# Optimization experiments

Hardware: AMD Instinct MI355X
Metric: run time of the kernel (lower is better)

## Reference

```python
import jax, jax.numpy as jnp
import numpy as np
from jax import lax

NX, NY, H = 128, 128, 1.0
N_ITER = 320          # ~2.5*(NX+NY): enough for one-cell-per-iter wavefront propagation
NUM_STATION = 24
NUM_EVENT = 2000
NUM_PICKS = 200000
INF = 1.0e6


def setup_inputs() -> dict:
    key = jax.random.key(0)
    ks = jax.random.split(key, 8)
    # velocities (km/s): vp ~ U[5,6], vs = vp/1.73 (Poisson solid)
    vp = 5.0 + jax.random.uniform(ks[0], (NX, NY), dtype=jnp.float32)
    vs = vp / 1.73
    scale = jnp.array([(NX - 1) * H, (NY - 1) * H, 0.0], dtype=jnp.float32)
    station_loc = jax.random.uniform(ks[1], (NUM_STATION, 3), dtype=jnp.float32) * scale
    event_loc = jax.random.uniform(ks[2], (NUM_EVENT, 3), dtype=jnp.float32) * scale
    event_time = jax.random.normal(ks[3], (NUM_EVENT, 1), dtype=jnp.float32)
    pick_station = jax.random.randint(ks[4], (NUM_PICKS,), 0, NUM_STATION)
    pick_phase = jax.random.randint(ks[5], (NUM_PICKS,), 0, 2)  # 0=P, 1=S
    pick_event = jax.random.randint(ks[6], (NUM_PICKS,), 0, NUM_EVENT)
    phase_time = 20.0 + jax.random.normal(ks[7], (NUM_PICKS,), dtype=jnp.float32)
    return dict(vp=vp, vs=vs, station_loc=station_loc, event_loc=event_loc,
                event_time=event_time, pick_station=pick_station,
                pick_phase=pick_phase, pick_event=pick_event, phase_time=phase_time)


def eikonal_solve(f, ix, iy):
    """2D eikonal |grad u| = f, point source at grid (ix,iy).
    Vectorized Jacobi iteration of the upwind Godunov local solver
    (same fixed point as the C++ fast-sweeping op)."""
    fh = f * H
    src = jnp.zeros((NX, NY), bool).at[ix, iy].set(True)
    u0 = jnp.where(src, 0.0, INF).astype(f.dtype)

    def body(u, _):
        up = jnp.pad(u, 1, constant_values=INF)
        a = jnp.minimum(up[:-2, 1:-1], up[2:, 1:-1])   # min x-neighbors
        b = jnp.minimum(up[1:-1, :-2], up[1:-1, 2:])   # min y-neighbors
        d = jnp.abs(a - b)
        one_sided = jnp.minimum(a, b) + fh
        two_sided = 0.5 * (a + b + jnp.sqrt(jnp.maximum(2.0 * fh * fh - d * d, 0.0)))
        cand = jnp.where(d >= fh, one_sided, two_sided)
        un = jnp.where(src, 0.0, jnp.minimum(u, cand))
        return un, None

    u, _ = lax.scan(body, u0, None, length=N_ITER)
    return u


def _forward(vp, vs, station_loc, event_loc, event_time,
             pick_station, pick_phase, pick_event, phase_time):
    # station grid indices: ix = round(station_x / h)
    ix = jnp.clip(jnp.round(station_loc[:, 0] / H), 0, NX - 1).astype(jnp.int32)
    iy = jnp.clip(jnp.round(station_loc[:, 1] / H), 0, NY - 1).astype(jnp.int32)
    solve_all = jax.vmap(eikonal_solve, in_axes=(None, 0, 0))
    Tp = solve_all(1.0 / vp, ix, iy)          # [S, NX, NY]
    Ts = solve_all(1.0 / vs, ix, iy)          # [S, NX, NY]
    T = jnp.stack([Tp, Ts])                    # [2, S, NX, NY]

    # bilinear interpolation of travel-time table at event locations (per pick)
    x = event_loc[pick_event, 0]
    y = event_loc[pick_event, 1]
    ir0 = jnp.clip(jnp.floor(x / H), 0, NX - 2).astype(jnp.int32)
    iz0 = jnp.clip(jnp.floor(y / H), 0, NY - 2).astype(jnp.int32)
    xc = jnp.clip(x, 0.0, (NX - 1) * H)
    yc = jnp.clip(y, 0.0, (NY - 1) * H)
    r0 = ir0.astype(xc.dtype) * H
    z0 = iz0.astype(yc.dtype) * H
    r1 = r0 + H
    z1 = z0 + H
    ph, st = pick_phase, pick_station
    Q00 = T[ph, st, ir0, iz0]
    Q01 = T[ph, st, ir0, iz0 + 1]
    Q10 = T[ph, st, ir0 + 1, iz0]
    Q11 = T[ph, st, ir0 + 1, iz0 + 1]
    tt = (Q00 * (r1 - xc) * (z1 - yc) + Q10 * (xc - r0) * (z1 - yc)
          + Q01 * (r1 - xc) * (yc - z0) + Q11 * (xc - r0) * (yc - z0)) / (H * H)

    at = event_time[pick_event, 0] + tt        # predicted arrival time, [NUM_PICKS]

    # loss = sum over (station, phase) groups of per-group MSE (matches groupby loop)
    gid = st * 2 + ph
    sq = (at - phase_time) ** 2
    sse = jax.ops.segment_sum(sq, gid, num_segments=2 * NUM_STATION)
    cnt = jax.ops.segment_sum(jnp.ones_like(sq), gid, num_segments=2 * NUM_STATION)
    loss = jnp.sum(sse / jnp.maximum(cnt, 1.0))
    return at, loss


def reference(vp, vs, station_loc, event_loc, event_time,
              pick_station, pick_phase, pick_event, phase_time):
    return _forward(vp, vs, station_loc, event_loc, event_time,
                    pick_station, pick_phase, pick_event, phase_time)
```

## Files before the change

### kernel.cpp

```cpp
#include <hip/hip_runtime.h>

#define NXg   128
#define NYg   128
#define NSTA  24
#define NPICK 200000
#define INFV  1.0e6f
#define TS    8
#define TG    16
#define MAXO  200

__device__ __forceinline__ float fsqrt_fast(float x) {
#if __has_builtin(__builtin_amdgcn_sqrtf)
  return __builtin_amdgcn_sqrtf(x);
#else
  float r; asm("v_sqrt_f32 %0, %1" : "=v"(r) : "v"(x)); return r;
#endif
}


template<int DR, int DC>
__device__ __forceinline__ void gs_pass(
    float (&u)[TS][TS], const float (&fh)[TS][TS], const float (&t2)[TS][TS],
    const float (&tpa)[TS], const float (&bta)[TS],
    const float (&lfa)[TS], const float (&rga)[TS], int &chg)
{
#pragma unroll
  for (int rr = 0; rr < TS; rr++) {
    const int r = (DR > 0) ? rr : (TS - 1 - rr);
#pragma unroll
    for (int cc = 0; cc < TS; cc++) {
      const int c = (DC > 0) ? cc : (TS - 1 - cc);
      const float up = (r == 0)      ? tpa[c] : u[r - 1][c];
      const float dn = (r == TS - 1) ? bta[c] : u[r + 1][c];
      const float lf = (c == 0)      ? lfa[r] : u[r][c - 1];
      const float rt = (c == TS - 1) ? rga[r] : u[r][c + 1];
      const float a  = fminf(up, dn);
      const float b  = fminf(lf, rt);
      const float dd = a - b;
      const float w  = fh[r][c];
      const float s  = fmaxf(__builtin_fmaf(-dd, dd, t2[r][c]), 0.0f);
      const float tw = 0.5f * ((a + b) + fsqrt_fast(s));
      const float on = fminf(a, b) + w;
      const float cand = (fabsf(dd) >= w) ? on : tw;
      const float old = u[r][c];
      chg |= (cand < old);
      u[r][c] = fminf(old, cand);
    }
  }
}

__global__ __launch_bounds__(256, 1) void eik_kernel(
    const float* __restrict__ vp, const float* __restrict__ vs,
    const float* __restrict__ station_loc, float* __restrict__ tab)
{
  __shared__ float eT[TG * TG][TS];
  __shared__ float eB[TG * TG][TS];
  __shared__ float eL[TG * TG][TS];
  __shared__ float eR[TG * TG][TS];
  __shared__ int flg[TG + 2][TG + 2];

  const int t    = threadIdx.x;
  const int wv   = t >> 6;
  const int lane = t & 63;
  const int ti = (wv >> 1) * 8 + (lane >> 3);
  const int tj = (wv & 1) * 8 + (lane & 7);
  const int tid = ti * TG + tj;
  const int fi = ti + 1, fj = tj + 1;

  const int blk = blockIdx.x;
  const int st = blk % NSTA;
  const int ph = blk / NSTA;
  const float* __restrict__ v = ph ? vs : vp;

  for (int i = t; i < (TG + 2) * (TG + 2); i += 256) {
    const int r = i / (TG + 2), c = i % (TG + 2);
    (&flg[0][0])[i] = (r >= 1 && r <= TG && c >= 1 && c <= TG) ? 1 : 0;
  }

  const float sx = station_loc[st * 3 + 0];
  const float sy = station_loc[st * 3 + 1];
  int ix = (int)rintf(sx); ix = ix < 0 ? 0 : (ix > NXg - 1 ? NXg - 1 : ix);
  int iy = (int)rintf(sy); iy = iy < 0 ? 0 : (iy > NYg - 1 ? NYg - 1 : iy);

  const int r0 = ti * TS, c0 = tj * TS;
  float u[TS][TS], fh[TS][TS], t2[TS][TS];
#pragma unroll
  for (int r = 0; r < TS; r++) {
    const float4 v0 = *reinterpret_cast<const float4*>(&v[(r0 + r) * NYg + c0]);
    const float4 v1 = *reinterpret_cast<const float4*>(&v[(r0 + r) * NYg + c0 + 4]);
    fh[r][0] = 1.0f / v0.x; fh[r][1] = 1.0f / v0.y;
    fh[r][2] = 1.0f / v0.z; fh[r][3] = 1.0f / v0.w;
    fh[r][4] = 1.0f / v1.x; fh[r][5] = 1.0f / v1.y;
    fh[r][6] = 1.0f / v1.z; fh[r][7] = 1.0f / v1.w;
#pragma unroll
    for (int c = 0; c < TS; c++) {
      t2[r][c] = (2.0f * fh[r][c]) * fh[r][c];
      u[r][c] = ((r0 + r) == ix && (c0 + c) == iy) ? 0.0f : INFV;
    }
  }

  auto publish = [&]() {
    *reinterpret_cast<float4*>(&eT[tid][0]) = make_float4(u[0][0], u[0][1], u[0][2], u[0][3]);
    *reinterpret_cast<float4*>(&eT[tid][4]) = make_float4(u[0][4], u[0][5], u[0][6], u[0][7]);
    *reinterpret_cast<float4*>(&eB[tid][0]) = make_float4(u[7][0], u[7][1], u[7][2], u[7][3]);
    *reinterpret_cast<float4*>(&eB[tid][4]) = make_float4(u[7][4], u[7][5], u[7][6], u[7][7]);
    *reinterpret_cast<float4*>(&eL[tid][0]) = make_float4(u[0][0], u[1][0], u[2][0], u[3][0]);
    *reinterpret_cast<float4*>(&eL[tid][4]) = make_float4(u[4][0], u[5][0], u[6][0], u[7][0]);
    *reinterpret_cast<float4*>(&eR[tid][0]) = make_float4(u[0][7], u[1][7], u[2][7], u[3][7]);
    *reinterpret_cast<float4*>(&eR[tid][4]) = make_float4(u[4][7], u[5][7], u[6][7], u[7][7]);
  };

  publish();
  __syncthreads();

  for (int outer = 0; outer < MAXO; outer++) {
    const int nb = flg[fi][fj]
                 | flg[fi - 1][fj] | flg[fi + 1][fj]
                 | flg[fi][fj - 1] | flg[fi][fj + 1];
    int chg = 0;
    if (__any(nb)) {
      float tpa[TS], bta[TS], lfa[TS], rga[TS];
      {
        float4 h0 = make_float4(INFV, INFV, INFV, INFV), h1 = h0;
        if (ti > 0) {
          h0 = *reinterpret_cast<const float4*>(&eB[tid - TG][0]);
          h1 = *reinterpret_cast<const float4*>(&eB[tid - TG][4]);
        }
        tpa[0] = h0.x; tpa[1] = h0.y; tpa[2] = h0.z; tpa[3] = h0.w;
        tpa[4] = h1.x; tpa[5] = h1.y; tpa[6] = h1.z; tpa[7] = h1.w;
      }
      {
        float4 h0 = make_float4(INFV, INFV, INFV, INFV), h1 = h0;
        if (ti < TG - 1) {
          h0 = *reinterpret_cast<const float4*>(&eT[tid + TG][0]);
          h1 = *reinterpret_cast<const float4*>(&eT[tid + TG][4]);
        }
        bta[0] = h0.x; bta[1] = h0.y; bta[2] = h0.z; bta[3] = h0.w;
        bta[4] = h1.x; bta[5] = h1.y; bta[6] = h1.z; bta[7] = h1.w;
      }
      {
        float4 h0 = make_float4(INFV, INFV, INFV, INFV), h1 = h0;
        if (tj > 0) {
          h0 = *reinterpret_cast<const float4*>(&eR[tid - 1][0]);
          h1 = *reinterpret_cast<const float4*>(&eR[tid - 1][4]);
        }
        lfa[0] = h0.x; lfa[1] = h0.y; lfa[2] = h0.z; lfa[3] = h0.w;
        lfa[4] = h1.x; lfa[5] = h1.y; lfa[6] = h1.z; lfa[7] = h1.w;
      }
      {
        float4 h0 = make_float4(INFV, INFV, INFV, INFV), h1 = h0;
        if (tj < TG - 1) {
          h0 = *reinterpret_cast<const float4*>(&eL[tid + 1][0]);
          h1 = *reinterpret_cast<const float4*>(&eL[tid + 1][4]);
        }
        rga[0] = h0.x; rga[1] = h0.y; rga[2] = h0.z; rga[3] = h0.w;
        rga[4] = h1.x; rga[5] = h1.y; rga[6] = h1.z; rga[7] = h1.w;
      }

      gs_pass<+1, +1>(u, fh, t2, tpa, bta, lfa, rga, chg);
      gs_pass<+1, -1>(u, fh, t2, tpa, bta, lfa, rga, chg);
      gs_pass<-1, +1>(u, fh, t2, tpa, bta, lfa, rga, chg);
      gs_pass<-1, -1>(u, fh, t2, tpa, bta, lfa, rga, chg);
    }

    __syncthreads();

    flg[fi][fj] = chg;
    if (chg) publish();

    if (!__syncthreads_or(chg)) break;
  }

  float* __restrict__ To = tab + (size_t)(ph * NSTA + st) * NXg * NYg;
#pragma unroll
  for (int r = 0; r < TS; r++) {
    *reinterpret_cast<float4*>(&To[(r0 + r) * NYg + c0]) =
        make_float4(u[r][0], u[r][1], u[r][2], u[r][3]);
    *reinterpret_cast<float4*>(&To[(r0 + r) * NYg + c0 + 4]) =
        make_float4(u[r][4], u[r][5], u[r][6], u[r][7]);
  }
}

__global__ void picks_kernel(
    const float* __restrict__ evloc, const float* __restrict__ evtime,
    const int* __restrict__ pst, const int* __restrict__ pph,
    const int* __restrict__ pev, const float* __restrict__ ptime,
    const float* __restrict__ tab, float* __restrict__ out,
    float* __restrict__ acc)
{
  __shared__ float lsse[2 * NSTA];
  __shared__ float lcnt[2 * NSTA];
  if (threadIdx.x < 2 * NSTA) { lsse[threadIdx.x] = 0.0f; lcnt[threadIdx.x] = 0.0f; }
  __syncthreads();

  int i = blockIdx.x * blockDim.x + threadIdx.x;
  if (i < NPICK) {
    int e = pev[i], s = pst[i], p = pph[i];
    float x = evloc[e * 3 + 0];
    float y = evloc[e * 3 + 1];
    int ir0 = (int)floorf(x); ir0 = ir0 < 0 ? 0 : (ir0 > NXg - 2 ? NXg - 2 : ir0);
    int iz0 = (int)floorf(y); iz0 = iz0 < 0 ? 0 : (iz0 > NYg - 2 ? NYg - 2 : iz0);
    float xc = fminf(fmaxf(x, 0.0f), (float)(NXg - 1));
    float yc = fminf(fmaxf(y, 0.0f), (float)(NYg - 1));
    float r0f = (float)ir0, z0f = (float)iz0;
    float r1 = r0f + 1.0f, z1 = z0f + 1.0f;

    const float* Tb = tab + (size_t)(p * NSTA + s) * NXg * NYg;
    float Q00 = Tb[ir0 * NYg + iz0];
    float Q01 = Tb[ir0 * NYg + iz0 + 1];
    float Q10 = Tb[(ir0 + 1) * NYg + iz0];
    float Q11 = Tb[(ir0 + 1) * NYg + iz0 + 1];
    float tt = Q00 * (r1 - xc) * (z1 - yc) + Q10 * (xc - r0f) * (z1 - yc)
             + Q01 * (r1 - xc) * (yc - z0f) + Q11 * (xc - r0f) * (yc - z0f);
    float at = evtime[e] + tt;
    out[i] = at;

    float dq = at - ptime[i];
    int g = s * 2 + p;
    atomicAdd(&lsse[g], dq * dq);
    atomicAdd(&lcnt[g], 1.0f);
  }
  __syncthreads();
  if (threadIdx.x < 2 * NSTA) {
    atomicAdd(&acc[threadIdx.x], lsse[threadIdx.x]);
    atomicAdd(&acc[2 * NSTA + threadIdx.x], lcnt[threadIdx.x]);
  }
}

__global__ void loss_kernel(const float* __restrict__ acc, float* __restrict__ out)
{
  int l = threadIdx.x;
  float v = 0.0f;
  if (l < 2 * NSTA) v = acc[l] / fmaxf(acc[2 * NSTA + l], 1.0f);
#pragma unroll
  for (int o = 32; o > 0; o >>= 1) v += __shfl_down(v, o, 64);
  if (l == 0) out[NPICK] = v;
}

extern "C" void kernel_launch(void* const* d_in, const int* in_sizes, int n_in,
                              void* d_out, int out_size, void* d_ws, size_t ws_size,
                              hipStream_t stream)
{
  const float* vp           = (const float*)d_in[0];
  const float* vs           = (const float*)d_in[1];
  const float* station_loc  = (const float*)d_in[2];
  const float* event_loc    = (const float*)d_in[3];
  const float* event_time   = (const float*)d_in[4];
  const int*   pick_station = (const int*)d_in[5];
  const int*   pick_phase   = (const int*)d_in[6];
  const int*   pick_event   = (const int*)d_in[7];
  const float* phase_time   = (const float*)d_in[8];

  float* out = (float*)d_out;
  float* acc = (float*)d_ws;
  float* tab = acc + 256;

  hipMemsetAsync(d_ws, 0, 96 * sizeof(float), stream);

  eik_kernel<<<2 * NSTA, 256, 0, stream>>>(vp, vs, station_loc, tab);

  picks_kernel<<<(NPICK + 255) / 256, 256, 0, stream>>>(
      event_loc, event_time, pick_station, pick_phase, pick_event, phase_time,
      tab, out, acc);

  loss_kernel<<<1, 64, 0, stream>>>(acc, out);
}
```

Measured before the change: 320.7 us.

## Split each tile iteration into two alternating sweep pairs with a two-iteration activity mask

Each outer iteration now runs two opposite-direction Gauss-Seidel sweeps instead of all four, alternating between the (+,+)/(-,-) and (+,-)/(-,+) pairs. Halo edges are therefore exchanged between tiles twice as often. A 2-bit history mask keeps a tile active if it or a neighbour changed in either of the last two iterations, and the change flag is only computed on the first sweep of each pair. The sqrt clamp is dropped because the one-sided branch is chosen whenever the argument could go negative. The aim is to spread the wavefront across tiles in fewer total sweeps, at the cost of more barriers and shared-memory publishes per sweep.

```diff
diff --git a/kernel.cpp b/kernel.cpp
--- a/kernel.cpp
+++ b/kernel.cpp
@@ -7,7 +7,7 @@
 #define INFV  1.0e6f
 #define TS    8
 #define TG    16
-#define MAXO  200
+#define MAXH  400
 
 __device__ __forceinline__ float fsqrt_fast(float x) {
 #if __has_builtin(__builtin_amdgcn_sqrtf)
@@ -18,7 +18,7 @@
 }
 
 
-template<int DR, int DC>
+template<int DR, int DC, bool CHK>
 __device__ __forceinline__ void gs_pass(
     float (&u)[TS][TS], const float (&fh)[TS][TS], const float (&t2)[TS][TS],
     const float (&tpa)[TS], const float (&bta)[TS],
@@ -38,12 +38,12 @@
       const float b  = fminf(lf, rt);
       const float dd = a - b;
       const float w  = fh[r][c];
-      const float s  = fmaxf(__builtin_fmaf(-dd, dd, t2[r][c]), 0.0f);
+      const float s  = __builtin_fmaf(-dd, dd, t2[r][c]);
       const float tw = 0.5f * ((a + b) + fsqrt_fast(s));
       const float on = fminf(a, b) + w;
       const float cand = (fabsf(dd) >= w) ? on : tw;
       const float old = u[r][c];
-      chg |= (cand < old);
+      if (CHK) chg |= (cand < old);
       u[r][c] = fminf(old, cand);
     }
   }
@@ -57,7 +57,7 @@
   __shared__ float eB[TG * TG][TS];
   __shared__ float eL[TG * TG][TS];
   __shared__ float eR[TG * TG][TS];
-  __shared__ int flg[TG + 2][TG + 2];
+  __shared__ int msk[TG + 2][TG + 2];
 
   const int t    = threadIdx.x;
   const int wv   = t >> 6;
@@ -74,7 +74,7 @@
 
   for (int i = t; i < (TG + 2) * (TG + 2); i += 256) {
     const int r = i / (TG + 2), c = i % (TG + 2);
-    (&flg[0][0])[i] = (r >= 1 && r <= TG && c >= 1 && c <= TG) ? 1 : 0;
+    (&msk[0][0])[i] = (r >= 1 && r <= TG && c >= 1 && c <= TG) ? 3 : 0;
   }
 
   const float sx = station_loc[st * 3 + 0];
@@ -113,12 +113,12 @@
   publish();
   __syncthreads();
 
-  for (int outer = 0; outer < MAXO; outer++) {
-    const int nb = flg[fi][fj]
-                 | flg[fi - 1][fj] | flg[fi + 1][fj]
-                 | flg[fi][fj - 1] | flg[fi][fj + 1];
+  for (int hg = 0; hg < MAXH; hg++) {
+    const int nbm = msk[fi][fj]
+                  | msk[fi - 1][fj] | msk[fi + 1][fj]
+                  | msk[fi][fj - 1] | msk[fi][fj + 1];
     int chg = 0;
-    if (__any(nb)) {
+    if (__any(nbm)) {
       float tpa[TS], bta[TS], lfa[TS], rga[TS];
       {
         float4 h0 = make_float4(INFV, INFV, INFV, INFV), h1 = h0;
@@ -157,15 +157,18 @@
         rga[4] = h1.x; rga[5] = h1.y; rga[6] = h1.z; rga[7] = h1.w;
       }
 
-      gs_pass<+1, +1>(u, fh, t2, tpa, bta, lfa, rga, chg);
-      gs_pass<+1, -1>(u, fh, t2, tpa, bta, lfa, rga, chg);
-      gs_pass<-1, +1>(u, fh, t2, tpa, bta, lfa, rga, chg);
-      gs_pass<-1, -1>(u, fh, t2, tpa, bta, lfa, rga, chg);
+      if ((hg & 1) == 0) {
+        gs_pass<+1, +1, true >(u, fh, t2, tpa, bta, lfa, rga, chg);
+        gs_pass<-1, -1, false>(u, fh, t2, tpa, bta, lfa, rga, chg);
+      } else {
+        gs_pass<+1, -1, true >(u, fh, t2, tpa, bta, lfa, rga, chg);
+        gs_pass<-1, +1, false>(u, fh, t2, tpa, bta, lfa, rga, chg);
+      }
     }
 
     __syncthreads();
 
-    flg[fi][fj] = chg;
+    msk[fi][fj] = ((msk[fi][fj] << 1) | chg) & 3;
     if (chg) publish();
 
     if (!__syncthreads_or(chg)) break;
```

Result: no change. 326.0 us (+1.7%).

## Order sweeps away from source per wave and skip passes once wave converges

Applied to the files above, without the earlier changes.

Each wave picks a Gauss-Seidel sweep order whose first pass runs away from the source, based on its quadrant relative to the source cell. After each directional pass the wave checks with __any whether anything changed and skips the remaining passes if not. The clamp before the sqrt is removed, since the two-sided branch is only selected when the argument is non-negative. This aims to cut redundant sweep work near convergence, at the cost of four unrolled code variants and a larger instruction footprint.

```diff
diff --git a/kernel.cpp b/kernel.cpp
--- a/kernel.cpp
+++ b/kernel.cpp
@@ -38,7 +38,7 @@
       const float b  = fminf(lf, rt);
       const float dd = a - b;
       const float w  = fh[r][c];
-      const float s  = fmaxf(__builtin_fmaf(-dd, dd, t2[r][c]), 0.0f);
+      const float s  = __builtin_fmaf(-dd, dd, t2[r][c]);
       const float tw = 0.5f * ((a + b) + fsqrt_fast(s));
       const float on = fminf(a, b) + w;
       const float cand = (fabsf(dd) >= w) ? on : tw;
@@ -49,6 +49,28 @@
   }
 }
 
+#define RUN4(R1,C1,R2,C2,R3,C3,R4,C4)                                   \
+  {                                                                     \
+    int c1 = 0;                                                         \
+    gs_pass<R1, C1>(u, fh, t2, tpa, bta, lfa, rga, c1);                 \
+    chg = c1;                                                           \
+    if (__any(c1)) {                                                    \
+      int c2 = 0;                                                       \
+      gs_pass<R2, C2>(u, fh, t2, tpa, bta, lfa, rga, c2);               \
+      chg |= c2;                                                        \
+      if (__any(c2)) {                                                  \
+        int c3 = 0;                                                     \
+        gs_pass<R3, C3>(u, fh, t2, tpa, bta, lfa, rga, c3);             \
+        chg |= c3;                                                      \
+        if (__any(c3)) {                                                \
+          int c4 = 0;                                                   \
+          gs_pass<R4, C4>(u, fh, t2, tpa, bta, lfa, rga, c4);           \
+          chg |= c4;                                                    \
+        }                                                               \
+      }                                                                 \
+    }                                                                   \
+  }
+
 __global__ __launch_bounds__(256, 1) void eik_kernel(
     const float* __restrict__ vp, const float* __restrict__ vs,
     const float* __restrict__ station_loc, float* __restrict__ tab)
@@ -81,6 +103,10 @@
   const float sy = station_loc[st * 3 + 1];
   int ix = (int)rintf(sx); ix = ix < 0 ? 0 : (ix > NXg - 1 ? NXg - 1 : ix);
   int iy = (int)rintf(sy); iy = iy < 0 ? 0 : (iy > NYg - 1 ? NYg - 1 : iy);
+
+  const int away_r = ((wv >> 1) * 64 + 32 > ix) ? 1 : 0;
+  const int away_c = ((wv & 1) * 64 + 32 > iy) ? 1 : 0;
+  const int order  = away_r * 2 + away_c;
 
   const int r0 = ti * TS, c0 = tj * TS;
   float u[TS][TS], fh[TS][TS], t2[TS][TS];
@@ -157,10 +183,12 @@
         rga[4] = h1.x; rga[5] = h1.y; rga[6] = h1.z; rga[7] = h1.w;
       }
 
-      gs_pass<+1, +1>(u, fh, t2, tpa, bta, lfa, rga, chg);
-      gs_pass<+1, -1>(u, fh, t2, tpa, bta, lfa, rga, chg);
-      gs_pass<-1, +1>(u, fh, t2, tpa, bta, lfa, rga, chg);
-      gs_pass<-1, -1>(u, fh, t2, tpa, bta, lfa, rga, chg);
+      switch (order) {
+        case 3: RUN4(+1, +1, +1, -1, -1, +1, -1, -1); break;
+        case 2: RUN4(+1, -1, +1, +1, -1, -1, -1, +1); break;
+        case 1: RUN4(-1, +1, -1, -1, +1, +1, +1, -1); break;
+        default:RUN4(-1, -1, -1, +1, +1, -1, +1, +1); break;
+      }
     }
 
     __syncthreads();
```

Result: no change. 319.3 us (-0.4%).
